# Kernel optimization log

Measured on AMD Instinct MI355X. Metric: run time of the kernel, lower is better.

The kernel has to match this reference:

```python
import jax, jax.numpy as jnp
import numpy as np

B, S, MSL, MQL = 512, 20, 32, 16
E, H, HQ = 32, 32, 32
V, A = 10000, 1000
D = H + S  # per-object feature dim (hidden + one-hot tag) = 52
G = 256


def _lstm_last_h(x, Wih, Whh, bih, bhh):
    # x: [N, T, E]; torch LSTM gate order i,f,g,o; returns final hidden [N, H]
    n, t, _ = x.shape
    h_dim = Whh.shape[1]
    xp = jnp.einsum('nte,ge->ntg', x, Wih) + bih + bhh  # precompute input projection

    def step(carry, xt):
        h, c = carry
        gates = xt + h @ Whh.T
        i, f, g, o = jnp.split(gates, 4, axis=-1)
        c = jax.nn.sigmoid(f) * c + jax.nn.sigmoid(i) * jnp.tanh(g)
        h = jax.nn.sigmoid(o) * jnp.tanh(c)
        return (h, c), None

    init = (jnp.zeros((n, h_dim), x.dtype), jnp.zeros((n, h_dim), x.dtype))
    (h, _), _ = jax.lax.scan(step, init, xp.transpose(1, 0, 2))
    return h


def setup_inputs() -> dict:
    key = jax.random.key(0)
    ks = jax.random.split(key, 24)
    nrm = lambda k, shp, std=0.1: (jax.random.normal(k, shp) * std).astype(jnp.float32)
    inp = {
        'story': jax.random.randint(ks[0], (B, S, MSL), 0, V),
        'question': jax.random.randint(ks[1], (B, MQL), 0, V),
        'emb': nrm(ks[2], (V, E)),
        's_Wih': nrm(ks[3], (4 * H, E)),
        's_Whh': nrm(ks[4], (4 * H, H)),
        's_bih': jnp.zeros((4 * H,), jnp.float32),
        's_bhh': jnp.zeros((4 * H,), jnp.float32),
        'q_Wih': nrm(ks[5], (4 * HQ, E)),
        'q_Whh': nrm(ks[6], (4 * HQ, HQ)),
        'q_bih': jnp.zeros((4 * HQ,), jnp.float32),
        'q_bhh': jnp.zeros((4 * HQ,), jnp.float32),
        'g1_w': nrm(ks[7], (G, 2 * D + HQ)), 'g1_b': jnp.zeros((G,), jnp.float32),
        'g2_w': nrm(ks[8], (G, G)), 'g2_b': jnp.zeros((G,), jnp.float32),
        'g3_w': nrm(ks[9], (G, G)), 'g3_b': jnp.zeros((G,), jnp.float32),
        'g4_w': nrm(ks[10], (G, G)), 'g4_b': jnp.zeros((G,), jnp.float32),
        'f1_w': nrm(ks[11], (G, G)), 'f1_b': jnp.zeros((G,), jnp.float32),
        'f2_w': nrm(ks[12], (512, G)), 'f2_b': jnp.zeros((512,), jnp.float32),
        'f3_w': nrm(ks[13], (A, 512)), 'f3_b': jnp.zeros((A,), jnp.float32),
    }
    return inp


def reference(story, question, emb, s_Wih, s_Whh, s_bih, s_bhh,
              q_Wih, q_Whh, q_bih, q_bhh,
              g1_w, g1_b, g2_w, g2_b, g3_w, g3_b, g4_w, g4_b,
              f1_w, f1_b, f2_w, f2_b, f3_w, f3_b):
    bsz = story.shape[0]
    # story encoding: LSTM over each sentence, take final hidden state
    s_emb = emb[story].reshape(bsz * S, MSL, E)
    s_state = _lstm_last_h(s_emb, s_Wih, s_Whh, s_bih, s_bhh).reshape(bsz, S, H)
    # append one-hot position tags -> story objects [B, S, H+S]
    tags = jnp.broadcast_to(jnp.eye(S, dtype=s_state.dtype), (bsz, S, S))
    obj = jnp.concatenate([s_state, tags], axis=2)
    # question encoding
    q_state = _lstm_last_h(emb[question], q_Wih, q_Whh, q_bih, q_bhh)  # [B, HQ]
    # g_theta over all S*S pairs: g1(cat(o_i, o_j, q)) split into three projections
    Wa, Wb, Wq = g1_w[:, :D], g1_w[:, D:2 * D], g1_w[:, 2 * D:]
    pi = jnp.einsum('bsd,gd->bsg', obj, Wa)   # object-as-first projection
    pj = jnp.einsum('bsd,gd->bsg', obj, Wb)   # object-as-second projection
    pq = q_state @ Wq.T                        # [B, G]
    x = jax.nn.relu(pi[:, :, None, :] + pj[:, None, :, :] + pq[:, None, None, :] + g1_b)  # [B,S,S,G]
    x = jax.nn.relu(jnp.einsum('bijg,hg->bijh', x, g2_w) + g2_b)
    x = jax.nn.relu(jnp.einsum('bijg,hg->bijh', x, g3_w) + g3_b)
    x = jax.nn.relu(jnp.einsum('bijg,hg->bijh', x, g4_w) + g4_b)
    sum_g = x.sum(axis=(1, 2))  # [B, G]
    out = jax.nn.relu(sum_g @ f1_w.T + f1_b)
    out = jax.nn.relu(out @ f2_w.T + f2_b)
    return out @ f3_w.T + f3_b
```

## Files before the change

### kernel.cpp

```cpp
#include <hip/hip_runtime.h>

typedef unsigned short u16;
typedef unsigned int   u32;
typedef __attribute__((ext_vector_type(8))) short short8;
typedef __attribute__((ext_vector_type(4))) float f32x4;

#define OFF_XPS   0
#define OFF_XPQ   1280000
#define OFF_QST   2560000
#define OFF_PI    2576384
#define OFF_PJ    5197824
#define OFF_QA    7819264
#define OFF_TGA   7950336
#define OFF_TGB   7955456
#define OFF_WB    7960576
#define OFF_STB   8058880
#define OFF_WAB   8222720
#define OFF_WBB   8226816
#define OFF_WHHS  8230912
#define OFF_WHHQ  8232960
#define OFF_WF1   8235008
#define OFF_WF2   8267776
#define OFF_WF3   8333312
#define OFF_SGP   0
#define OFF_ACT1  720896
#define OFF_ACT2  786432

__device__ __forceinline__ u16 f2bf(float f){
  union { float f; u32 u; } v; v.f = f;
  u32 u = v.u;
  u32 r = u + 0x7fffu + ((u >> 16) & 1u);
  return (u16)(r >> 16);
}
__device__ __forceinline__ u32 pack2(float a, float b){
  u32 r;
  asm("v_cvt_pk_bf16_f32 %0, %1, %2" : "=v"(r) : "v"(a), "v"(b));
  return r;
}
__device__ __forceinline__ float sigm(float x){
  return __builtin_amdgcn_rcpf(1.f + __expf(-x));
}

#define LBAR() do {                                        \
    asm volatile("s_waitcnt lgkmcnt(0)" ::: "memory");     \
    __builtin_amdgcn_s_barrier();                          \
    __builtin_amdgcn_sched_barrier(0);                     \
  } while (0)

__global__ __launch_bounds__(256) void prep_kernel(
    const float* __restrict__ emb,
    const float* __restrict__ swih, const float* __restrict__ sbih, const float* __restrict__ sbhh,
    const float* __restrict__ qwih, const float* __restrict__ qbih, const float* __restrict__ qbhh,
    const float* __restrict__ g2w, const float* __restrict__ g3w, const float* __restrict__ g4w,
    const float* __restrict__ g1w,
    const float* __restrict__ swhh, const float* __restrict__ qwhh,
    const float* __restrict__ f1w, const float* __restrict__ f2w, const float* __restrict__ f3w,
    float* __restrict__ xps, float* __restrict__ xpq,
    u16* __restrict__ wb, u16* __restrict__ wab, u16* __restrict__ wbb,
    float* __restrict__ tga, float* __restrict__ tgb,
    u16* __restrict__ whhbs, u16* __restrict__ whhbq,
    u16* __restrict__ wf1, u16* __restrict__ wf2, u16* __restrict__ wf3)
{
  __shared__ float wl[2048];
  __shared__ float bl[64];
  const int tid = threadIdx.x;
  if (blockIdx.y == 2){
    const int B = 196608;
    const int C = B + 16384;
    const int D = C + 10240;
    const int E = D + 8192;
    const int F = E + 65536;
    const int G = F + 131072;
    const int H = G + 524288;
    for (int idx = blockIdx.x*256 + tid; idx < H; idx += 160*256){
      if (idx < B){
        const int k = idx;
        const float* src = (k < 65536) ? g2w : ((k < 131072) ? g3w : g4w);
        wb[k] = f2bf(src[k & 65535]);
      } else if (idx < C){
        const int k = idx - B;
        if (k < 8192) wab[k] = f2bf(g1w[(k>>5)*136 + (k&31)]);
        else { const int k2 = k - 8192; wbb[k2] = f2bf(g1w[(k2>>5)*136 + 52 + (k2&31)]); }
      } else if (idx < D){
        const int k = idx - C;
        if (k < 5120){ const int s = k >> 8, g = k & 255; tga[k] = g1w[g*136 + 32 + s]; }
        else { const int k2 = k - 5120; const int s = k2 >> 8, g = k2 & 255; tgb[k2] = g1w[g*136 + 84 + s]; }
      } else if (idx < E){
        const int k = idx - D;
        if (k < 4096) whhbs[k] = f2bf(swhh[k]);
        else whhbq[k-4096] = f2bf(qwhh[k-4096]);
      } else if (idx < F){
        const int k = idx - E;
        wf1[k] = f2bf(f1w[k]);
      } else if (idx < G){
        const int k = idx - F;
        wf2[k] = f2bf(f2w[k]);
      } else {
        const int k = idx - G;
        const int o = k >> 9, kk = k & 511;
        wf3[k] = (o < 1000) ? f2bf(f3w[o*512 + kk]) : (u16)0;
      }
    }
    return;
  }
  if (blockIdx.x >= 80) return;
  const bool isq = blockIdx.y;
  const float* wih = isq ? qwih : swih;
  const float* bih = isq ? qbih : sbih;
  const float* bhh = isq ? qbhh : sbhh;
  float* xp = isq ? xpq : xps;
  const int gh = (blockIdx.x & 1) * 64;
  #pragma unroll
  for (int k=0;k<8;k++) wl[k*256+tid] = wih[gh*32 + k*256 + tid];
  if (tid < 64) bl[tid] = bih[gh+tid] + bhh[gh+tid];
  __syncthreads();
  const int v = (blockIdx.x >> 1)*256 + tid;
  if (v >= 10000) return;
  float4 e[8];
  #pragma unroll
  for (int q=0;q<8;q++) e[q] = *(const float4*)(emb + v*32 + q*4);
  for (int g2=0; g2<64; ++g2){
    const int g = gh + g2;
    float acc = bl[g2];
    #pragma unroll
    for (int q=0;q<8;q++){
      float4 w4 = *(const float4*)(&wl[g2*32 + q*4]);
      acc = fmaf(e[q].x, w4.x, acc); acc = fmaf(e[q].y, w4.y, acc);
      acc = fmaf(e[q].z, w4.z, acc); acc = fmaf(e[q].w, w4.w, acc);
    }
    xp[v*128 + (g&15)*8 + (g>>4)] = acc;
  }
}

template<int LEN>
__device__ __forceinline__ void lstm_mfma_run(
    const int* __restrict__ toks, int s0,
    const float* __restrict__ xpr, const u16* __restrict__ whhb,
    u16* __restrict__ hl, int lane, float* h0r, float* h1r)
{
  const int l15 = lane & 15, l4 = lane >> 4;
  short8 wf[8];
  #pragma unroll
  for (int f=0; f<8; f++)
    wf[f] = *(const short8*)(whhb + (f*16+l15)*32 + l4*8);
  short8 ha = (short8){0,0,0,0,0,0,0,0};
  float c0[4] = {0,0,0,0}, c1[4] = {0,0,0,0};
  int tk[4];
  #pragma unroll
  for (int r=0;r<4;r++) tk[r] = toks[(s0 + l4*4 + r)*LEN];
  float4 xa[4], xb[4];
  #pragma unroll
  for (int r=0;r<4;r++){
    xa[r] = *(const float4*)(xpr + tk[r]*128 + l15*8);
    xb[r] = *(const float4*)(xpr + tk[r]*128 + l15*8 + 4);
  }
  #pragma unroll
  for (int t=0; t<LEN; ++t){
    int tkn[4];
    if (t+1 < LEN){
      #pragma unroll
      for (int r=0;r<4;r++) tkn[r] = toks[(s0 + l4*4 + r)*LEN + t + 1];
    }
    const f32x4 z = (f32x4){0.f,0.f,0.f,0.f};
    f32x4 acc[8];
    #pragma unroll
    for (int f=0; f<8; f++)
      acc[f] = __builtin_amdgcn_mfma_f32_16x16x32_bf16(ha, wf[f], z, 0, 0, 0);
    float4 na[4], nb[4];
    if (t+1 < LEN){
      #pragma unroll
      for (int r=0;r<4;r++){
        na[r] = *(const float4*)(xpr + tkn[r]*128 + l15*8);
        nb[r] = *(const float4*)(xpr + tkn[r]*128 + l15*8 + 4);
      }
    }
    #pragma unroll
    for (int r=0;r<4;r++){
      float i0 = sigm(acc[0][r] + xa[r].x);
      float f0 = sigm(acc[2][r] + xa[r].z);
      float g0 = 2.f*sigm(2.f*(acc[4][r] + xb[r].x)) - 1.f;
      float o0 = sigm(acc[6][r] + xb[r].z);
      c0[r] = fmaf(f0, c0[r], i0*g0);
      h0r[r] = o0 * (2.f*sigm(2.f*c0[r]) - 1.f);
      float i1 = sigm(acc[1][r] + xa[r].y);
      float f1v = sigm(acc[3][r] + xa[r].w);
      float g1v = 2.f*sigm(2.f*(acc[5][r] + xb[r].y)) - 1.f;
      float o1 = sigm(acc[7][r] + xb[r].w);
      c1[r] = fmaf(f1v, c1[r], i1*g1v);
      h1r[r] = o1 * (2.f*sigm(2.f*c1[r]) - 1.f);
    }
    if (t+1 < LEN){
      #pragma unroll
      for (int r=0;r<4;r++){
        hl[(l4*4+r)*32 + l15]      = f2bf(h0r[r]);
        hl[(l4*4+r)*32 + 16 + l15] = f2bf(h1r[r]);
      }
      __syncthreads();
      ha = *(const short8*)(hl + l15*32 + l4*8);
      #pragma unroll
      for (int r=0;r<4;r++){ xa[r] = na[r]; xb[r] = nb[r]; }
    }
  }
}

__global__ __launch_bounds__(64) void lstm_kernel(
    const int* __restrict__ story, const int* __restrict__ question,
    const float* __restrict__ xprs, const float* __restrict__ xprq,
    const u16* __restrict__ whhbs, const u16* __restrict__ whhbq,
    u16* __restrict__ stb, float* __restrict__ qst)
{
  __shared__ u16 hl[512];
  const int lane = threadIdx.x;
  const int w = blockIdx.x;
  const int l15 = lane & 15, l4 = lane >> 4;
  float h0r[4], h1r[4];
  if (w >= 640){
    const int s0 = (w - 640)*16;
    lstm_mfma_run<16>(question, s0, xprq, whhbq, hl, lane, h0r, h1r);
    #pragma unroll
    for (int r=0;r<4;r++){
      qst[(s0 + l4*4 + r)*32 + l15]      = h0r[r];
      qst[(s0 + l4*4 + r)*32 + 16 + l15] = h1r[r];
    }
  } else {
    const int s0 = w*16;
    lstm_mfma_run<32>(story, s0, xprs, whhbs, hl, lane, h0r, h1r);
    #pragma unroll
    for (int r=0;r<4;r++){
      stb[(s0 + l4*4 + r)*32 + l15]      = f2bf(h0r[r]);
      stb[(s0 + l4*4 + r)*32 + 16 + l15] = f2bf(h1r[r]);
    }
  }
}

__global__ __launch_bounds__(256) void pipj_kernel(
    const u16* __restrict__ stb, const u16* __restrict__ wab, const u16* __restrict__ wbb,
    const float* __restrict__ tga, const float* __restrict__ tgb,
    const float* __restrict__ qst, const float* __restrict__ g1w, const float* __restrict__ g1b,
    float* __restrict__ pi, float* __restrict__ pj, float* __restrict__ qa)
{
  const int tid = threadIdx.x;
  if (blockIdx.y == 2){
    for (int idx = blockIdx.x*256 + tid; idx < 131072; idx += 160*256){
      const int b = idx >> 8, g = idx & 255;
      const float* qs = qst + b*32;
      const float* wr = g1w + g*136 + 104;
      float acc = g1b[g];
      #pragma unroll
      for (int q=0;q<8;q++){
        float4 s4 = *(const float4*)(qs + q*4);
        float4 w4 = *(const float4*)(wr + q*4);
        acc = fmaf(s4.x, w4.x, acc); acc = fmaf(s4.y, w4.y, acc);
        acc = fmaf(s4.z, w4.z, acc); acc = fmaf(s4.w, w4.w, acc);
      }
      qa[idx] = acc;
    }
    return;
  }
  const int lane = tid & 63;
  const int wv = tid >> 6;
  const int l15 = lane & 15;
  const int l4r = lane >> 4;
  const int bs0 = blockIdx.x * 64;
  const bool isj = blockIdx.y;
  const u16* wB = isj ? wbb : wab;
  const float* tg = isj ? tgb : tga;
  float* out = isj ? pj : pi;

  short8 af[4], bf[4];
  #pragma unroll
  for (int mf=0; mf<4; mf++)
    af[mf] = *(const short8*)(stb + (bs0 + mf*16 + l15)*32 + l4r*8);
  #pragma unroll
  for (int nf=0; nf<4; nf++)
    bf[nf] = *(const short8*)(wB + (wv*64 + nf*16 + l15)*32 + l4r*8);

  #pragma unroll
  for (int mf=0; mf<4; mf++){
    #pragma unroll
    for (int nf=0; nf<4; nf++){
      f32x4 acc = (f32x4){0.f,0.f,0.f,0.f};
      acc = __builtin_amdgcn_mfma_f32_16x16x32_bf16(af[mf], bf[nf], acc, 0, 0, 0);
      const int g = wv*64 + nf*16 + l15;
      #pragma unroll
      for (int r=0; r<4; r++){
        const int bs = bs0 + mf*16 + l4r*4 + r;
        const int s = bs % 20;
        out[bs*256 + g] = acc[r] + tg[s*256 + g];
      }
    }
  }
}

#define LDX 264
__global__ __launch_bounds__(512) void relnet_kernel(
    const float* __restrict__ pi, const float* __restrict__ pj, const float* __restrict__ qa,
    const u16* __restrict__ w2, const u16* __restrict__ w3, const u16* __restrict__ w4,
    const float* __restrict__ b2, const float* __restrict__ b3, const float* __restrict__ b4,
    float* __restrict__ sgp)
{
  __shared__ u16 Xs[80*LDX + 6656];
  const int tid = threadIdx.x;
  const int lane = tid & 63;
  const int wv  = tid >> 6;
  const int b   = blockIdx.x;
  const int t   = blockIdx.y;
  const int l15 = lane & 15;
  const int l4  = lane >> 4;

  const float* pib = pi + b*(20*256);
  const float* pjb = pj + b*(20*256);
  const float* qab = qa + b*256;

  const int ar0 = (wv*32 + l15)*256 + l4*8;
  const int ar1 = (wv*32 + 16 + l15)*256 + l4*8;

  #pragma unroll
  for (int it = 0; it < 5; ++it){
    int u  = it*512 + tid;
    int m  = u >> 5;
    int gq = (u & 31) << 3;
    int R  = t*80 + m;
    int i  = R / 20;
    int j  = R - i*20;
    const float4* pr = (const float4*)(pib + i*256 + gq);
    const float4* qr = (const float4*)(pjb + j*256 + gq);
    const float4* ar = (const float4*)(qab + gq);
    uint4 pk;
    {
      float4 a = pr[0], c4 = qr[0], d4 = ar[0];
      pk.x = pack2(fmaxf(a.x+c4.x+d4.x,0.f), fmaxf(a.y+c4.y+d4.y,0.f));
      pk.y = pack2(fmaxf(a.z+c4.z+d4.z,0.f), fmaxf(a.w+c4.w+d4.w,0.f));
    }
    {
      float4 a = pr[1], c4 = qr[1], d4 = ar[1];
      pk.z = pack2(fmaxf(a.x+c4.x+d4.x,0.f), fmaxf(a.y+c4.y+d4.y,0.f));
      pk.w = pack2(fmaxf(a.z+c4.z+d4.z,0.f), fmaxf(a.w+c4.w+d4.w,0.f));
    }
    *(uint4*)(&Xs[m*LDX + gq]) = pk;
  }

  short8 pf0 = *(const short8*)(w2 + ar0);
  short8 pf1 = *(const short8*)(w2 + ar1);

  LBAR();

  #pragma unroll
  for (int lay = 0; lay < 2; ++lay){
    const u16*   W    = lay ? w3 : w2;
    const u16*   Wn   = lay ? w4 : w3;
    const float* bias = lay ? b3 : b2;
    f32x4 acc[2][5];
    #pragma unroll
    for (int hf=0; hf<2; hf++)
      #pragma unroll
      for (int mf=0; mf<5; mf++)
        acc[hf][mf] = (f32x4){0.f,0.f,0.f,0.f};

    short8 xc[5];
    #pragma unroll
    for (int mf=0; mf<5; mf++)
      xc[mf] = *(const short8*)(&Xs[(mf*16 + l15)*LDX + l4*8]);

    #pragma unroll
    for (int kk = 0; kk < 8; ++kk){
      short8 a0 = pf0, a1 = pf1;
      const u16* src = (kk < 7) ? W : Wn;
      const int  kn  = (kk < 7) ? (kk+1)*32 : 0;
      pf0 = *(const short8*)(src + ar0 + kn);
      pf1 = *(const short8*)(src + ar1 + kn);
      short8 xn[5];
      if (kk < 7){
        #pragma unroll
        for (int mf=0; mf<5; mf++)
          xn[mf] = *(const short8*)(&Xs[(mf*16 + l15)*LDX + (kk+1)*32 + l4*8]);
      }
      __builtin_amdgcn_s_setprio(1);
      #pragma unroll
      for (int mf=0; mf<5; mf++){
        acc[0][mf] = __builtin_amdgcn_mfma_f32_16x16x32_bf16(a0, xc[mf], acc[0][mf], 0, 0, 0);
        acc[1][mf] = __builtin_amdgcn_mfma_f32_16x16x32_bf16(a1, xc[mf], acc[1][mf], 0, 0, 0);
      }
      __builtin_amdgcn_s_setprio(0);
      if (kk < 7){
        #pragma unroll
        for (int mf=0; mf<5; mf++) xc[mf] = xn[mf];
      }
    }

    LBAR();
    #pragma unroll
    for (int hf=0; hf<2; hf++){
      int h0 = wv*32 + hf*16 + l4*4;
      float4 bi = *(const float4*)(bias + h0);
      #pragma unroll
      for (int mf=0; mf<5; mf++){
        int m = mf*16 + l15;
        uint2 pk;
        pk.x = pack2(fmaxf(acc[hf][mf][0]+bi.x,0.f), fmaxf(acc[hf][mf][1]+bi.y,0.f));
        pk.y = pack2(fmaxf(acc[hf][mf][2]+bi.z,0.f), fmaxf(acc[hf][mf][3]+bi.w,0.f));
        *(uint2*)(&Xs[m*LDX + h0]) = pk;
      }
    }
    LBAR();
  }

  {
    f32x4 acc[2][5];
    #pragma unroll
    for (int hf=0; hf<2; hf++)
      #pragma unroll
      for (int mf=0; mf<5; mf++)
        acc[hf][mf] = (f32x4){0.f,0.f,0.f,0.f};

    short8 xc[5];
    #pragma unroll
    for (int mf=0; mf<5; mf++)
      xc[mf] = *(const short8*)(&Xs[(mf*16 + l15)*LDX + l4*8]);

    #pragma unroll
    for (int kk = 0; kk < 8; ++kk){
      short8 a0 = pf0, a1 = pf1;
      if (kk < 7){
        pf0 = *(const short8*)(w4 + ar0 + (kk+1)*32);
        pf1 = *(const short8*)(w4 + ar1 + (kk+1)*32);
      }
      short8 xn[5];
      if (kk < 7){
        #pragma unroll
        for (int mf=0; mf<5; mf++)
          xn[mf] = *(const short8*)(&Xs[(mf*16 + l15)*LDX + (kk+1)*32 + l4*8]);
      }
      __builtin_amdgcn_s_setprio(1);
      #pragma unroll
      for (int mf=0; mf<5; mf++){
        acc[0][mf] = __builtin_amdgcn_mfma_f32_16x16x32_bf16(a0, xc[mf], acc[0][mf], 0, 0, 0);
        acc[1][mf] = __builtin_amdgcn_mfma_f32_16x16x32_bf16(a1, xc[mf], acc[1][mf], 0, 0, 0);
      }
      __builtin_amdgcn_s_setprio(0);
      if (kk < 7){
        #pragma unroll
        for (int mf=0; mf<5; mf++) xc[mf] = xn[mf];
      }
    }

    #pragma unroll
    for (int hf=0; hf<2; hf++){
      int h0 = wv*32 + hf*16 + l4*4;
      float4 bi = *(const float4*)(b4 + h0);
      float s0 = 0.f, s1 = 0.f, s2 = 0.f, s3 = 0.f;
      #pragma unroll
      for (int mf=0; mf<5; mf++){
        s0 += fmaxf(acc[hf][mf][0]+bi.x,0.f);
        s1 += fmaxf(acc[hf][mf][1]+bi.y,0.f);
        s2 += fmaxf(acc[hf][mf][2]+bi.z,0.f);
        s3 += fmaxf(acc[hf][mf][3]+bi.w,0.f);
      }
      float sv[4] = {s0, s1, s2, s3};
      #pragma unroll
      for (int r=0; r<4; r++){
        float v = sv[r];
        v += __shfl_xor(v, 1);
        v += __shfl_xor(v, 2);
        v += __shfl_xor(v, 4);
        v += __shfl_xor(v, 8);
        if (l15 == 0){
          int h = h0 + r;
          sgp[t*131072 + b*256 + h] = v;
        }
      }
    }
  }
}

__global__ __launch_bounds__(256) void fcm1_kernel(
    const float* __restrict__ sgp, const u16* __restrict__ w,
    const float* __restrict__ bias, u16* __restrict__ outp)
{
  const int tid = threadIdx.x, lane = tid & 63, wv = tid >> 6;
  const int l15 = lane & 15, l4 = lane >> 4;
  const int b0 = blockIdx.x*16;
  const int of0 = blockIdx.y*4 + wv;
  f32x4 acc = (f32x4){0.f,0.f,0.f,0.f};
  #pragma unroll
  for (int kk=0; kk<8; ++kk){
    const float* base = sgp + (b0+l15)*256 + kk*32 + l4*8;
    float4 s0 = {0.f,0.f,0.f,0.f}, s1 = {0.f,0.f,0.f,0.f};
    #pragma unroll
    for (int t=0;t<5;t++){
      float4 a = *(const float4*)(base + t*131072);
      float4 c = *(const float4*)(base + t*131072 + 4);
      s0.x += a.x; s0.y += a.y; s0.z += a.z; s0.w += a.w;
      s1.x += c.x; s1.y += c.y; s1.z += c.z; s1.w += c.w;
    }
    union { short8 s; u32 u[4]; } xf;
    xf.u[0] = pack2(s0.x, s0.y); xf.u[1] = pack2(s0.z, s0.w);
    xf.u[2] = pack2(s1.x, s1.y); xf.u[3] = pack2(s1.z, s1.w);
    short8 af = *(const short8*)(w + (of0*16 + l15)*256 + kk*32 + l4*8);
    acc = __builtin_amdgcn_mfma_f32_16x16x32_bf16(af, xf.s, acc, 0, 0, 0);
  }
  const int b = b0 + l15;
  const int o0 = of0*16 + l4*4;
  float v0 = fmaxf(acc[0] + bias[o0+0], 0.f);
  float v1 = fmaxf(acc[1] + bias[o0+1], 0.f);
  float v2 = fmaxf(acc[2] + bias[o0+2], 0.f);
  float v3 = fmaxf(acc[3] + bias[o0+3], 0.f);
  uint2 pk;
  pk.x = pack2(v0, v1);
  pk.y = pack2(v2, v3);
  *(uint2*)(outp + (size_t)b*256 + o0) = pk;
}

template<int HF, int KK, int OPAD, int OREAL, int MODE>
__global__ __launch_bounds__(256) void fcm_kernel(
    const u16* __restrict__ in, const u16* __restrict__ w,
    const float* __restrict__ bias, void* __restrict__ outp)
{
  const int K = KK*32;
  const int tid = threadIdx.x, lane = tid & 63, wv = tid >> 6;
  const int l15 = lane & 15, l4 = lane >> 4;
  const int b0 = blockIdx.x*16;
  const int of0 = (blockIdx.y*4 + wv)*HF;
  f32x4 acc[HF];
  #pragma unroll
  for (int hf=0; hf<HF; hf++) acc[hf] = (f32x4){0.f,0.f,0.f,0.f};
  #pragma unroll 4
  for (int kk=0; kk<KK; ++kk){
    short8 xf = *(const short8*)(in + (b0+l15)*K + kk*32 + l4*8);
    #pragma unroll
    for (int hf=0; hf<HF; hf++){
      short8 af = *(const short8*)(w + ((of0+hf)*16 + l15)*K + kk*32 + l4*8);
      acc[hf] = __builtin_amdgcn_mfma_f32_16x16x32_bf16(af, xf, acc[hf], 0, 0, 0);
    }
  }
  const int b = b0 + l15;
  #pragma unroll
  for (int hf=0; hf<HF; hf++){
    const int o0 = (of0+hf)*16 + l4*4;
    float v[4];
    #pragma unroll
    for (int r=0;r<4;r++){
      float bv = (o0+r < OREAL) ? bias[o0+r] : 0.f;
      v[r] = acc[hf][r] + bv;
    }
    if (MODE == 0){
      uint2 pk;
      pk.x = pack2(fmaxf(v[0],0.f), fmaxf(v[1],0.f));
      pk.y = pack2(fmaxf(v[2],0.f), fmaxf(v[3],0.f));
      *(uint2*)((u16*)outp + (size_t)b*OPAD + o0) = pk;
    } else {
      float* of = (float*)outp;
      #pragma unroll
      for (int r=0;r<4;r++)
        if (o0+r < OREAL) of[(size_t)b*OREAL + o0 + r] = v[r];
    }
  }
}

extern "C" void kernel_launch(void* const* d_in, const int* in_sizes, int n_in,
                              void* d_out, int out_size, void* d_ws, size_t ws_size,
                              hipStream_t stream)
{
  const int*   story    = (const int*)d_in[0];
  const int*   question = (const int*)d_in[1];
  const float* emb   = (const float*)d_in[2];
  const float* s_wih = (const float*)d_in[3];
  const float* s_whh = (const float*)d_in[4];
  const float* s_bih = (const float*)d_in[5];
  const float* s_bhh = (const float*)d_in[6];
  const float* q_wih = (const float*)d_in[7];
  const float* q_whh = (const float*)d_in[8];
  const float* q_bih = (const float*)d_in[9];
  const float* q_bhh = (const float*)d_in[10];
  const float* g1w = (const float*)d_in[11];
  const float* g1b = (const float*)d_in[12];
  const float* g2w = (const float*)d_in[13];
  const float* g2b = (const float*)d_in[14];
  const float* g3w = (const float*)d_in[15];
  const float* g3b = (const float*)d_in[16];
  const float* g4w = (const float*)d_in[17];
  const float* g4b = (const float*)d_in[18];
  const float* f1w = (const float*)d_in[19];
  const float* f1b = (const float*)d_in[20];
  const float* f2w = (const float*)d_in[21];
  const float* f2b = (const float*)d_in[22];
  const float* f3w = (const float*)d_in[23];
  const float* f3b = (const float*)d_in[24];

  float* ws  = (float*)d_ws;
  float* xps = ws + OFF_XPS;
  float* xpq = ws + OFF_XPQ;
  float* qst = ws + OFF_QST;
  float* pi  = ws + OFF_PI;
  float* pj  = ws + OFF_PJ;
  float* qa  = ws + OFF_QA;
  float* tga = ws + OFF_TGA;
  float* tgb = ws + OFF_TGB;
  float* sgp = ws + OFF_SGP;
  u16*   wb    = (u16*)(ws + OFF_WB);
  u16*   w2b   = wb;
  u16*   w3b   = wb + 65536;
  u16*   w4b   = wb + 131072;
  u16*   stb   = (u16*)(ws + OFF_STB);
  u16*   wab   = (u16*)(ws + OFF_WAB);
  u16*   wbb   = (u16*)(ws + OFF_WBB);
  u16*   whhbs = (u16*)(ws + OFF_WHHS);
  u16*   whhbq = (u16*)(ws + OFF_WHHQ);
  u16*   wf1   = (u16*)(ws + OFF_WF1);
  u16*   wf2   = (u16*)(ws + OFF_WF2);
  u16*   wf3   = (u16*)(ws + OFF_WF3);
  u16*   act1  = (u16*)(ws + OFF_ACT1);
  u16*   act2  = (u16*)(ws + OFF_ACT2);

  prep_kernel<<<dim3(160,3), dim3(256), 0, stream>>>(
      emb, s_wih, s_bih, s_bhh, q_wih, q_bih, q_bhh,
      g2w, g3w, g4w, g1w, s_whh, q_whh, f1w, f2w, f3w,
      xps, xpq, wb, wab, wbb, tga, tgb, whhbs, whhbq, wf1, wf2, wf3);
  lstm_kernel<<<dim3(672), dim3(64), 0, stream>>>(
      story, question, xps, xpq, whhbs, whhbq, stb, qst);
  pipj_kernel<<<dim3(160,3), dim3(256), 0, stream>>>(
      stb, wab, wbb, tga, tgb, qst, g1w, g1b, pi, pj, qa);
  relnet_kernel<<<dim3(512,5), dim3(512), 0, stream>>>(
      pi, pj, qa, w2b, w3b, w4b, g2b, g3b, g4b, sgp);
  fcm1_kernel<<<dim3(32,4), dim3(256), 0, stream>>>(sgp, wf1, f1b, act1);
  fcm_kernel<2,8,512,512,0><<<dim3(32,4), dim3(256), 0, stream>>>(act1, wf2, f2b, act2);
  fcm_kernel<2,16,1024,1000,1><<<dim3(32,8), dim3(256), 0, stream>>>(act2, wf3, f3b, (float*)d_out);
}
```

Before: 231.6 us.

## Process two batch items per relnet block to reuse weight fragments

Each relnet block now handles two batch elements, with two shared-memory activation tiles and two accumulator sets, so every weight fragment loaded from global memory feeds twice as many MFMAs. The grid is halved to match. The old cross-layer weight prefetch and s_setprio hints are dropped, so weight loads are now issued inside each k-step. The extra accumulators raise register pressure and may lower occupancy, and halving the block count leaves fewer blocks for latency hiding.

Measured after the change: 202.7 us. -12.5%, faster.

```diff
diff --git a/kernel.cpp b/kernel.cpp
--- a/kernel.cpp
+++ b/kernel.cpp
@@ -299,92 +299,83 @@
     const float* __restrict__ b2, const float* __restrict__ b3, const float* __restrict__ b4,
     float* __restrict__ sgp)
 {
-  __shared__ u16 Xs[80*LDX + 6656];
+  __shared__ u16 Xs[2][80*LDX];
   const int tid = threadIdx.x;
   const int lane = tid & 63;
   const int wv  = tid >> 6;
-  const int b   = blockIdx.x;
+  const int bA  = blockIdx.x*2;
   const int t   = blockIdx.y;
   const int l15 = lane & 15;
   const int l4  = lane >> 4;
 
-  const float* pib = pi + b*(20*256);
-  const float* pjb = pj + b*(20*256);
-  const float* qab = qa + b*256;
-
   const int ar0 = (wv*32 + l15)*256 + l4*8;
   const int ar1 = (wv*32 + 16 + l15)*256 + l4*8;
 
   #pragma unroll
-  for (int it = 0; it < 5; ++it){
-    int u  = it*512 + tid;
-    int m  = u >> 5;
-    int gq = (u & 31) << 3;
-    int R  = t*80 + m;
-    int i  = R / 20;
-    int j  = R - i*20;
-    const float4* pr = (const float4*)(pib + i*256 + gq);
-    const float4* qr = (const float4*)(pjb + j*256 + gq);
-    const float4* ar = (const float4*)(qab + gq);
-    uint4 pk;
-    {
-      float4 a = pr[0], c4 = qr[0], d4 = ar[0];
-      pk.x = pack2(fmaxf(a.x+c4.x+d4.x,0.f), fmaxf(a.y+c4.y+d4.y,0.f));
-      pk.y = pack2(fmaxf(a.z+c4.z+d4.z,0.f), fmaxf(a.w+c4.w+d4.w,0.f));
-    }
-    {
-      float4 a = pr[1], c4 = qr[1], d4 = ar[1];
-      pk.z = pack2(fmaxf(a.x+c4.x+d4.x,0.f), fmaxf(a.y+c4.y+d4.y,0.f));
-      pk.w = pack2(fmaxf(a.z+c4.z+d4.z,0.f), fmaxf(a.w+c4.w+d4.w,0.f));
-    }
-    *(uint4*)(&Xs[m*LDX + gq]) = pk;
-  }
-
-  short8 pf0 = *(const short8*)(w2 + ar0);
-  short8 pf1 = *(const short8*)(w2 + ar1);
-
+  for (int s = 0; s < 2; ++s){
+    const float* pib = pi + (bA+s)*(20*256);
+    const float* pjb = pj + (bA+s)*(20*256);
+    const float* qab = qa + (bA+s)*256;
+    #pragma unroll
+    for (int it = 0; it < 5; ++it){
+      int u  = it*512 + tid;
+      int m  = u >> 5;
+      int gq = (u & 31) << 3;
+      int R  = t*80 + m;
+      int i  = R / 20;
+      int j  = R - i*20;
+      const float4* pr = (const float4*)(pib + i*256 + gq);
+      const float4* qr = (const float4*)(pjb + j*256 + gq);
+      const float4* ar = (const float4*)(qab + gq);
+      uint4 pk;
+      {
+        float4 a = pr[0], c4 = qr[0], d4 = ar[0];
+        pk.x = pack2(fmaxf(a.x+c4.x+d4.x,0.f), fmaxf(a.y+c4.y+d4.y,0.f));
+        pk.y = pack2(fmaxf(a.z+c4.z+d4.z,0.f), fmaxf(a.w+c4.w+d4.w,0.f));
+      }
+      {
+        float4 a = pr[1], c4 = qr[1], d4 = ar[1];
+        pk.z = pack2(fmaxf(a.x+c4.x+d4.x,0.f), fmaxf(a.y+c4.y+d4.y,0.f));
+        pk.w = pack2(fmaxf(a.z+c4.z+d4.z,0.f), fmaxf(a.w+c4.w+d4.w,0.f));
+      }
+      *(uint4*)(&Xs[s][m*LDX + gq]) = pk;
+    }
+  }
   LBAR();
 
   #pragma unroll
   for (int lay = 0; lay < 2; ++lay){
     const u16*   W    = lay ? w3 : w2;
-    const u16*   Wn   = lay ? w4 : w3;
     const float* bias = lay ? b3 : b2;
-    f32x4 acc[2][5];
+    f32x4 aA[2][5], aB[2][5];
     #pragma unroll
     for (int hf=0; hf<2; hf++)
       #pragma unroll
+      for (int mf=0; mf<5; mf++){
+        aA[hf][mf] = (f32x4){0.f,0.f,0.f,0.f};
+        aB[hf][mf] = (f32x4){0.f,0.f,0.f,0.f};
+      }
+
+    #pragma unroll
+    for (int kk = 0; kk < 8; ++kk){
+      short8 w0 = *(const short8*)(W + ar0 + kk*32);
+      short8 w1 = *(const short8*)(W + ar1 + kk*32);
+      short8 xA[5], xB[5];
+      #pragma unroll
       for (int mf=0; mf<5; mf++)
-        acc[hf][mf] = (f32x4){0.f,0.f,0.f,0.f};
-
-    short8 xc[5];
-    #pragma unroll
-    for (int mf=0; mf<5; mf++)
-      xc[mf] = *(const short8*)(&Xs[(mf*16 + l15)*LDX + l4*8]);
-
-    #pragma unroll
-    for (int kk = 0; kk < 8; ++kk){
-      short8 a0 = pf0, a1 = pf1;
-      const u16* src = (kk < 7) ? W : Wn;
-      const int  kn  = (kk < 7) ? (kk+1)*32 : 0;
-      pf0 = *(const short8*)(src + ar0 + kn);
-      pf1 = *(const short8*)(src + ar1 + kn);
-      short8 xn[5];
-      if (kk < 7){
-        #pragma unroll
-        for (int mf=0; mf<5; mf++)
-          xn[mf] = *(const short8*)(&Xs[(mf*16 + l15)*LDX + (kk+1)*32 + l4*8]);
-      }
-      __builtin_amdgcn_s_setprio(1);
-      #pragma unroll
-      for (int mf=0; mf<5; mf++){
-        acc[0][mf] = __builtin_amdgcn_mfma_f32_16x16x32_bf16(a0, xc[mf], acc[0][mf], 0, 0, 0);
-        acc[1][mf] = __builtin_amdgcn_mfma_f32_16x16x32_bf16(a1, xc[mf], acc[1][mf], 0, 0, 0);
-      }
-      __builtin_amdgcn_s_setprio(0);
-      if (kk < 7){
-        #pragma unroll
-        for (int mf=0; mf<5; mf++) xc[mf] = xn[mf];
+        xA[mf] = *(const short8*)(&Xs[0][(mf*16 + l15)*LDX + kk*32 + l4*8]);
+      #pragma unroll
+      for (int mf=0; mf<5; mf++)
+        xB[mf] = *(const short8*)(&Xs[1][(mf*16 + l15)*LDX + kk*32 + l4*8]);
+      #pragma unroll
+      for (int mf=0; mf<5; mf++){
+        aA[0][mf] = __builtin_amdgcn_mfma_f32_16x16x32_bf16(w0, xA[mf], aA[0][mf], 0, 0, 0);
+        aA[1][mf] = __builtin_amdgcn_mfma_f32_16x16x32_bf16(w1, xA[mf], aA[1][mf], 0, 0, 0);
+      }
+      #pragma unroll
+      for (int mf=0; mf<5; mf++){
+        aB[0][mf] = __builtin_amdgcn_mfma_f32_16x16x32_bf16(w0, xB[mf], aB[0][mf], 0, 0, 0);
+        aB[1][mf] = __builtin_amdgcn_mfma_f32_16x16x32_bf16(w1, xB[mf], aB[1][mf], 0, 0, 0);
       }
     }
 
@@ -396,51 +387,48 @@
       #pragma unroll
       for (int mf=0; mf<5; mf++){
         int m = mf*16 + l15;
-        uint2 pk;
-        pk.x = pack2(fmaxf(acc[hf][mf][0]+bi.x,0.f), fmaxf(acc[hf][mf][1]+bi.y,0.f));
-        pk.y = pack2(fmaxf(acc[hf][mf][2]+bi.z,0.f), fmaxf(acc[hf][mf][3]+bi.w,0.f));
-        *(uint2*)(&Xs[m*LDX + h0]) = pk;
+        uint2 pkA, pkB;
+        pkA.x = pack2(fmaxf(aA[hf][mf][0]+bi.x,0.f), fmaxf(aA[hf][mf][1]+bi.y,0.f));
+        pkA.y = pack2(fmaxf(aA[hf][mf][2]+bi.z,0.f), fmaxf(aA[hf][mf][3]+bi.w,0.f));
+        *(uint2*)(&Xs[0][m*LDX + h0]) = pkA;
+        pkB.x = pack2(fmaxf(aB[hf][mf][0]+bi.x,0.f), fmaxf(aB[hf][mf][1]+bi.y,0.f));
+        pkB.y = pack2(fmaxf(aB[hf][mf][2]+bi.z,0.f), fmaxf(aB[hf][mf][3]+bi.w,0.f));
+        *(uint2*)(&Xs[1][m*LDX + h0]) = pkB;
       }
     }
     LBAR();
   }
 
   {
-    f32x4 acc[2][5];
+    f32x4 aA[2][5], aB[2][5];
     #pragma unroll
     for (int hf=0; hf<2; hf++)
       #pragma unroll
+      for (int mf=0; mf<5; mf++){
+        aA[hf][mf] = (f32x4){0.f,0.f,0.f,0.f};
+        aB[hf][mf] = (f32x4){0.f,0.f,0.f,0.f};
+      }
+
+    #pragma unroll
+    for (int kk = 0; kk < 8; ++kk){
+      short8 w0 = *(const short8*)(w4 + ar0 + kk*32);
+      short8 w1 = *(const short8*)(w4 + ar1 + kk*32);
+      short8 xA[5], xB[5];
+      #pragma unroll
       for (int mf=0; mf<5; mf++)
-        acc[hf][mf] = (f32x4){0.f,0.f,0.f,0.f};
-
-    short8 xc[5];
-    #pragma unroll
-    for (int mf=0; mf<5; mf++)
-      xc[mf] = *(const short8*)(&Xs[(mf*16 + l15)*LDX + l4*8]);
-
-    #pragma unroll
-    for (int kk = 0; kk < 8; ++kk){
-      short8 a0 = pf0, a1 = pf1;
-      if (kk < 7){
-        pf0 = *(const short8*)(w4 + ar0 + (kk+1)*32);
-        pf1 = *(const short8*)(w4 + ar1 + (kk+1)*32);
-      }
-      short8 xn[5];
-      if (kk < 7){
-        #pragma unroll
-        for (int mf=0; mf<5; mf++)
-          xn[mf] = *(const short8*)(&Xs[(mf*16 + l15)*LDX + (kk+1)*32 + l4*8]);
-      }
-      __builtin_amdgcn_s_setprio(1);
-      #pragma unroll
-      for (int mf=0; mf<5; mf++){
-        acc[0][mf] = __builtin_amdgcn_mfma_f32_16x16x32_bf16(a0, xc[mf], acc[0][mf], 0, 0, 0);
-        acc[1][mf] = __builtin_amdgcn_mfma_f32_16x16x32_bf16(a1, xc[mf], acc[1][mf], 0, 0, 0);
-      }
-      __builtin_amdgcn_s_setprio(0);
-      if (kk < 7){
-        #pragma unroll
-        for (int mf=0; mf<5; mf++) xc[mf] = xn[mf];
+        xA[mf] = *(const short8*)(&Xs[0][(mf*16 + l15)*LDX + kk*32 + l4*8]);
+      #pragma unroll
+      for (int mf=0; mf<5; mf++)
+        xB[mf] = *(const short8*)(&Xs[1][(mf*16 + l15)*LDX + kk*32 + l4*8]);
+      #pragma unroll
+      for (int mf=0; mf<5; mf++){
+        aA[0][mf] = __builtin_amdgcn_mfma_f32_16x16x32_bf16(w0, xA[mf], aA[0][mf], 0, 0, 0);
+        aA[1][mf] = __builtin_amdgcn_mfma_f32_16x16x32_bf16(w1, xA[mf], aA[1][mf], 0, 0, 0);
+      }
+      #pragma unroll
+      for (int mf=0; mf<5; mf++){
+        aB[0][mf] = __builtin_amdgcn_mfma_f32_16x16x32_bf16(w0, xB[mf], aB[0][mf], 0, 0, 0);
+        aB[1][mf] = __builtin_amdgcn_mfma_f32_16x16x32_bf16(w1, xB[mf], aB[1][mf], 0, 0, 0);
       }
     }
 
@@ -448,25 +436,35 @@
     for (int hf=0; hf<2; hf++){
       int h0 = wv*32 + hf*16 + l4*4;
       float4 bi = *(const float4*)(b4 + h0);
-      float s0 = 0.f, s1 = 0.f, s2 = 0.f, s3 = 0.f;
-      #pragma unroll
-      for (int mf=0; mf<5; mf++){
-        s0 += fmaxf(acc[hf][mf][0]+bi.x,0.f);
-        s1 += fmaxf(acc[hf][mf][1]+bi.y,0.f);
-        s2 += fmaxf(acc[hf][mf][2]+bi.z,0.f);
-        s3 += fmaxf(acc[hf][mf][3]+bi.w,0.f);
-      }
-      float sv[4] = {s0, s1, s2, s3};
+      float sA[4] = {0.f,0.f,0.f,0.f};
+      float sB[4] = {0.f,0.f,0.f,0.f};
+      #pragma unroll
+      for (int mf=0; mf<5; mf++){
+        sA[0] += fmaxf(aA[hf][mf][0]+bi.x,0.f);
+        sA[1] += fmaxf(aA[hf][mf][1]+bi.y,0.f);
+        sA[2] += fmaxf(aA[hf][mf][2]+bi.z,0.f);
+        sA[3] += fmaxf(aA[hf][mf][3]+bi.w,0.f);
+        sB[0] += fmaxf(aB[hf][mf][0]+bi.x,0.f);
+        sB[1] += fmaxf(aB[hf][mf][1]+bi.y,0.f);
+        sB[2] += fmaxf(aB[hf][mf][2]+bi.z,0.f);
+        sB[3] += fmaxf(aB[hf][mf][3]+bi.w,0.f);
+      }
       #pragma unroll
       for (int r=0; r<4; r++){
-        float v = sv[r];
-        v += __shfl_xor(v, 1);
-        v += __shfl_xor(v, 2);
-        v += __shfl_xor(v, 4);
-        v += __shfl_xor(v, 8);
+        float vA = sA[r];
+        vA += __shfl_xor(vA, 1);
+        vA += __shfl_xor(vA, 2);
+        vA += __shfl_xor(vA, 4);
+        vA += __shfl_xor(vA, 8);
+        float vB = sB[r];
+        vB += __shfl_xor(vB, 1);
+        vB += __shfl_xor(vB, 2);
+        vB += __shfl_xor(vB, 4);
+        vB += __shfl_xor(vB, 8);
         if (l15 == 0){
           int h = h0 + r;
-          sgp[t*131072 + b*256 + h] = v;
+          sgp[t*131072 + bA*256 + h]       = vA;
+          sgp[t*131072 + (bA+1)*256 + h]   = vB;
         }
       }
     }
@@ -620,7 +618,7 @@
       story, question, xps, xpq, whhbs, whhbq, stb, qst);
   pipj_kernel<<<dim3(160,3), dim3(256), 0, stream>>>(
       stb, wab, wbb, tga, tgb, qst, g1w, g1b, pi, pj, qa);
-  relnet_kernel<<<dim3(512,5), dim3(512), 0, stream>>>(
+  relnet_kernel<<<dim3(256,5), dim3(512), 0, stream>>>(
       pi, pj, qa, w2b, w3b, w4b, g2b, g3b, g4b, sgp);
   fcm1_kernel<<<dim3(32,4), dim3(256), 0, stream>>>(sgp, wf1, f1b, act1);
   fcm_kernel<2,8,512,512,0><<<dim3(32,4), dim3(256), 0, stream>>>(act1, wf2, f2b, act2);
```

## Process all pair tiles per batch in one block to reuse weight fragments

Applied to the files above, without the earlier changes.

The relation-network kernel now launches one block per batch element instead of five. Each block handles the 400 pairs in two passes of three and two 80-row tiles. Each weight fragment loaded from global memory is reused across several tiles, cutting redundant weight traffic. The cost is fewer blocks (512 versus 2560), more LDS per block (three tiles), more accumulator registers (up to 120 f32x4 per thread), and loss of the software prefetch and setprio scheduling, so occupancy and latency hiding may drop.

Result: faster. 205.8 us (-11.2%).

```diff
diff --git a/kernel.cpp b/kernel.cpp
--- a/kernel.cpp
+++ b/kernel.cpp
@@ -293,184 +293,181 @@
 }
 
 #define LDX 264
+#define TSZ (80*LDX)
+
+template<int NT>
+__device__ __forceinline__ void relnet_pass(
+    int b, int t0, u16* __restrict__ Xs,
+    const float* __restrict__ pi, const float* __restrict__ pj, const float* __restrict__ qa,
+    const u16* __restrict__ w2, const u16* __restrict__ w3, const u16* __restrict__ w4,
+    const float* __restrict__ b2, const float* __restrict__ b3, const float* __restrict__ b4,
+    float* __restrict__ sgp,
+    int tid, int wv, int l15, int l4, int ar0, int ar1)
+{
+  const float* pib = pi + b*(20*256);
+  const float* pjb = pj + b*(20*256);
+  const float* qab = qa + b*256;
+
+  #pragma unroll
+  for (int s = 0; s < NT; ++s){
+    const int tt = t0 + s;
+    #pragma unroll
+    for (int it = 0; it < 5; ++it){
+      int ux = it*512 + tid;
+      int m  = ux >> 5;
+      int gq = (ux & 31) << 3;
+      int R  = tt*80 + m;
+      int i  = R / 20;
+      int j  = R - i*20;
+      const float4* pr = (const float4*)(pib + i*256 + gq);
+      const float4* qr = (const float4*)(pjb + j*256 + gq);
+      const float4* ar = (const float4*)(qab + gq);
+      uint4 pk;
+      {
+        float4 a = pr[0], c4 = qr[0], d4 = ar[0];
+        pk.x = pack2(fmaxf(a.x+c4.x+d4.x,0.f), fmaxf(a.y+c4.y+d4.y,0.f));
+        pk.y = pack2(fmaxf(a.z+c4.z+d4.z,0.f), fmaxf(a.w+c4.w+d4.w,0.f));
+      }
+      {
+        float4 a = pr[1], c4 = qr[1], d4 = ar[1];
+        pk.z = pack2(fmaxf(a.x+c4.x+d4.x,0.f), fmaxf(a.y+c4.y+d4.y,0.f));
+        pk.w = pack2(fmaxf(a.z+c4.z+d4.z,0.f), fmaxf(a.w+c4.w+d4.w,0.f));
+      }
+      *(uint4*)(&Xs[s*TSZ + m*LDX + gq]) = pk;
+    }
+  }
+  LBAR();
+
+  #pragma unroll
+  for (int lay = 0; lay < 2; ++lay){
+    const u16*   W    = lay ? w3 : w2;
+    const float* bias = lay ? b3 : b2;
+    f32x4 acc[NT][2][5];
+    #pragma unroll
+    for (int s=0; s<NT; s++)
+      #pragma unroll
+      for (int hf=0; hf<2; hf++)
+        #pragma unroll
+        for (int mf=0; mf<5; mf++)
+          acc[s][hf][mf] = (f32x4){0.f,0.f,0.f,0.f};
+
+    #pragma unroll
+    for (int kk = 0; kk < 8; ++kk){
+      short8 w0 = *(const short8*)(W + ar0 + kk*32);
+      short8 w1 = *(const short8*)(W + ar1 + kk*32);
+      #pragma unroll
+      for (int s=0; s<NT; s++){
+        short8 xf[5];
+        #pragma unroll
+        for (int mf=0; mf<5; mf++)
+          xf[mf] = *(const short8*)(&Xs[s*TSZ + (mf*16 + l15)*LDX + kk*32 + l4*8]);
+        #pragma unroll
+        for (int mf=0; mf<5; mf++){
+          acc[s][0][mf] = __builtin_amdgcn_mfma_f32_16x16x32_bf16(w0, xf[mf], acc[s][0][mf], 0, 0, 0);
+          acc[s][1][mf] = __builtin_amdgcn_mfma_f32_16x16x32_bf16(w1, xf[mf], acc[s][1][mf], 0, 0, 0);
+        }
+      }
+    }
+
+    LBAR();
+    #pragma unroll
+    for (int hf=0; hf<2; hf++){
+      int h0 = wv*32 + hf*16 + l4*4;
+      float4 bi = *(const float4*)(bias + h0);
+      #pragma unroll
+      for (int mf=0; mf<5; mf++){
+        int m = mf*16 + l15;
+        #pragma unroll
+        for (int s=0; s<NT; s++){
+          uint2 pk;
+          pk.x = pack2(fmaxf(acc[s][hf][mf][0]+bi.x,0.f), fmaxf(acc[s][hf][mf][1]+bi.y,0.f));
+          pk.y = pack2(fmaxf(acc[s][hf][mf][2]+bi.z,0.f), fmaxf(acc[s][hf][mf][3]+bi.w,0.f));
+          *(uint2*)(&Xs[s*TSZ + m*LDX + h0]) = pk;
+        }
+      }
+    }
+    LBAR();
+  }
+
+  {
+    f32x4 acc[NT][2][5];
+    #pragma unroll
+    for (int s=0; s<NT; s++)
+      #pragma unroll
+      for (int hf=0; hf<2; hf++)
+        #pragma unroll
+        for (int mf=0; mf<5; mf++)
+          acc[s][hf][mf] = (f32x4){0.f,0.f,0.f,0.f};
+
+    #pragma unroll
+    for (int kk = 0; kk < 8; ++kk){
+      short8 w0 = *(const short8*)(w4 + ar0 + kk*32);
+      short8 w1 = *(const short8*)(w4 + ar1 + kk*32);
+      #pragma unroll
+      for (int s=0; s<NT; s++){
+        short8 xf[5];
+        #pragma unroll
+        for (int mf=0; mf<5; mf++)
+          xf[mf] = *(const short8*)(&Xs[s*TSZ + (mf*16 + l15)*LDX + kk*32 + l4*8]);
+        #pragma unroll
+        for (int mf=0; mf<5; mf++){
+          acc[s][0][mf] = __builtin_amdgcn_mfma_f32_16x16x32_bf16(w0, xf[mf], acc[s][0][mf], 0, 0, 0);
+          acc[s][1][mf] = __builtin_amdgcn_mfma_f32_16x16x32_bf16(w1, xf[mf], acc[s][1][mf], 0, 0, 0);
+        }
+      }
+    }
+
+    #pragma unroll
+    for (int hf=0; hf<2; hf++){
+      int h0 = wv*32 + hf*16 + l4*4;
+      float4 bi = *(const float4*)(b4 + h0);
+      #pragma unroll
+      for (int s=0; s<NT; s++){
+        float s0 = 0.f, s1 = 0.f, s2 = 0.f, s3 = 0.f;
+        #pragma unroll
+        for (int mf=0; mf<5; mf++){
+          s0 += fmaxf(acc[s][hf][mf][0]+bi.x,0.f);
+          s1 += fmaxf(acc[s][hf][mf][1]+bi.y,0.f);
+          s2 += fmaxf(acc[s][hf][mf][2]+bi.z,0.f);
+          s3 += fmaxf(acc[s][hf][mf][3]+bi.w,0.f);
+        }
+        float sv[4] = {s0, s1, s2, s3};
+        #pragma unroll
+        for (int r=0; r<4; r++){
+          float v = sv[r];
+          v += __shfl_xor(v, 1); v += __shfl_xor(v, 2);
+          v += __shfl_xor(v, 4); v += __shfl_xor(v, 8);
+          if (l15 == 0){
+            int h = h0 + r;
+            sgp[(t0+s)*131072 + b*256 + h] = v;
+          }
+        }
+      }
+    }
+  }
+}
+
 __global__ __launch_bounds__(512) void relnet_kernel(
     const float* __restrict__ pi, const float* __restrict__ pj, const float* __restrict__ qa,
     const u16* __restrict__ w2, const u16* __restrict__ w3, const u16* __restrict__ w4,
     const float* __restrict__ b2, const float* __restrict__ b3, const float* __restrict__ b4,
     float* __restrict__ sgp)
 {
-  __shared__ u16 Xs[80*LDX + 6656];
+  __shared__ u16 Xs[3*TSZ];
   const int tid = threadIdx.x;
   const int lane = tid & 63;
   const int wv  = tid >> 6;
-  const int b   = blockIdx.x;
-  const int t   = blockIdx.y;
   const int l15 = lane & 15;
   const int l4  = lane >> 4;
-
-  const float* pib = pi + b*(20*256);
-  const float* pjb = pj + b*(20*256);
-  const float* qab = qa + b*256;
-
+  const int b   = blockIdx.x;
   const int ar0 = (wv*32 + l15)*256 + l4*8;
   const int ar1 = (wv*32 + 16 + l15)*256 + l4*8;
 
-  #pragma unroll
-  for (int it = 0; it < 5; ++it){
-    int u  = it*512 + tid;
-    int m  = u >> 5;
-    int gq = (u & 31) << 3;
-    int R  = t*80 + m;
-    int i  = R / 20;
-    int j  = R - i*20;
-    const float4* pr = (const float4*)(pib + i*256 + gq);
-    const float4* qr = (const float4*)(pjb + j*256 + gq);
-    const float4* ar = (const float4*)(qab + gq);
-    uint4 pk;
-    {
-      float4 a = pr[0], c4 = qr[0], d4 = ar[0];
-      pk.x = pack2(fmaxf(a.x+c4.x+d4.x,0.f), fmaxf(a.y+c4.y+d4.y,0.f));
-      pk.y = pack2(fmaxf(a.z+c4.z+d4.z,0.f), fmaxf(a.w+c4.w+d4.w,0.f));
-    }
-    {
-      float4 a = pr[1], c4 = qr[1], d4 = ar[1];
-      pk.z = pack2(fmaxf(a.x+c4.x+d4.x,0.f), fmaxf(a.y+c4.y+d4.y,0.f));
-      pk.w = pack2(fmaxf(a.z+c4.z+d4.z,0.f), fmaxf(a.w+c4.w+d4.w,0.f));
-    }
-    *(uint4*)(&Xs[m*LDX + gq]) = pk;
-  }
-
-  short8 pf0 = *(const short8*)(w2 + ar0);
-  short8 pf1 = *(const short8*)(w2 + ar1);
-
+  relnet_pass<3>(b, 0, Xs, pi, pj, qa, w2, w3, w4, b2, b3, b4, sgp,
+                 tid, wv, l15, l4, ar0, ar1);
   LBAR();
-
-  #pragma unroll
-  for (int lay = 0; lay < 2; ++lay){
-    const u16*   W    = lay ? w3 : w2;
-    const u16*   Wn   = lay ? w4 : w3;
-    const float* bias = lay ? b3 : b2;
-    f32x4 acc[2][5];
-    #pragma unroll
-    for (int hf=0; hf<2; hf++)
-      #pragma unroll
-      for (int mf=0; mf<5; mf++)
-        acc[hf][mf] = (f32x4){0.f,0.f,0.f,0.f};
-
-    short8 xc[5];
-    #pragma unroll
-    for (int mf=0; mf<5; mf++)
-      xc[mf] = *(const short8*)(&Xs[(mf*16 + l15)*LDX + l4*8]);
-
-    #pragma unroll
-    for (int kk = 0; kk < 8; ++kk){
-      short8 a0 = pf0, a1 = pf1;
-      const u16* src = (kk < 7) ? W : Wn;
-      const int  kn  = (kk < 7) ? (kk+1)*32 : 0;
-      pf0 = *(const short8*)(src + ar0 + kn);
-      pf1 = *(const short8*)(src + ar1 + kn);
-      short8 xn[5];
-      if (kk < 7){
-        #pragma unroll
-        for (int mf=0; mf<5; mf++)
-          xn[mf] = *(const short8*)(&Xs[(mf*16 + l15)*LDX + (kk+1)*32 + l4*8]);
-      }
-      __builtin_amdgcn_s_setprio(1);
-      #pragma unroll
-      for (int mf=0; mf<5; mf++){
-        acc[0][mf] = __builtin_amdgcn_mfma_f32_16x16x32_bf16(a0, xc[mf], acc[0][mf], 0, 0, 0);
-        acc[1][mf] = __builtin_amdgcn_mfma_f32_16x16x32_bf16(a1, xc[mf], acc[1][mf], 0, 0, 0);
-      }
-      __builtin_amdgcn_s_setprio(0);
-      if (kk < 7){
-        #pragma unroll
-        for (int mf=0; mf<5; mf++) xc[mf] = xn[mf];
-      }
-    }
-
-    LBAR();
-    #pragma unroll
-    for (int hf=0; hf<2; hf++){
-      int h0 = wv*32 + hf*16 + l4*4;
-      float4 bi = *(const float4*)(bias + h0);
-      #pragma unroll
-      for (int mf=0; mf<5; mf++){
-        int m = mf*16 + l15;
-        uint2 pk;
-        pk.x = pack2(fmaxf(acc[hf][mf][0]+bi.x,0.f), fmaxf(acc[hf][mf][1]+bi.y,0.f));
-        pk.y = pack2(fmaxf(acc[hf][mf][2]+bi.z,0.f), fmaxf(acc[hf][mf][3]+bi.w,0.f));
-        *(uint2*)(&Xs[m*LDX + h0]) = pk;
-      }
-    }
-    LBAR();
-  }
-
-  {
-    f32x4 acc[2][5];
-    #pragma unroll
-    for (int hf=0; hf<2; hf++)
-      #pragma unroll
-      for (int mf=0; mf<5; mf++)
-        acc[hf][mf] = (f32x4){0.f,0.f,0.f,0.f};
-
-    short8 xc[5];
-    #pragma unroll
-    for (int mf=0; mf<5; mf++)
-      xc[mf] = *(const short8*)(&Xs[(mf*16 + l15)*LDX + l4*8]);
-
-    #pragma unroll
-    for (int kk = 0; kk < 8; ++kk){
-      short8 a0 = pf0, a1 = pf1;
-      if (kk < 7){
-        pf0 = *(const short8*)(w4 + ar0 + (kk+1)*32);
-        pf1 = *(const short8*)(w4 + ar1 + (kk+1)*32);
-      }
-      short8 xn[5];
-      if (kk < 7){
-        #pragma unroll
-        for (int mf=0; mf<5; mf++)
-          xn[mf] = *(const short8*)(&Xs[(mf*16 + l15)*LDX + (kk+1)*32 + l4*8]);
-      }
-      __builtin_amdgcn_s_setprio(1);
-      #pragma unroll
-      for (int mf=0; mf<5; mf++){
-        acc[0][mf] = __builtin_amdgcn_mfma_f32_16x16x32_bf16(a0, xc[mf], acc[0][mf], 0, 0, 0);
-        acc[1][mf] = __builtin_amdgcn_mfma_f32_16x16x32_bf16(a1, xc[mf], acc[1][mf], 0, 0, 0);
-      }
-      __builtin_amdgcn_s_setprio(0);
-      if (kk < 7){
-        #pragma unroll
-        for (int mf=0; mf<5; mf++) xc[mf] = xn[mf];
-      }
-    }
-
-    #pragma unroll
-    for (int hf=0; hf<2; hf++){
-      int h0 = wv*32 + hf*16 + l4*4;
-      float4 bi = *(const float4*)(b4 + h0);
-      float s0 = 0.f, s1 = 0.f, s2 = 0.f, s3 = 0.f;
-      #pragma unroll
-      for (int mf=0; mf<5; mf++){
-        s0 += fmaxf(acc[hf][mf][0]+bi.x,0.f);
-        s1 += fmaxf(acc[hf][mf][1]+bi.y,0.f);
-        s2 += fmaxf(acc[hf][mf][2]+bi.z,0.f);
-        s3 += fmaxf(acc[hf][mf][3]+bi.w,0.f);
-      }
-      float sv[4] = {s0, s1, s2, s3};
-      #pragma unroll
-      for (int r=0; r<4; r++){
-        float v = sv[r];
-        v += __shfl_xor(v, 1);
-        v += __shfl_xor(v, 2);
-        v += __shfl_xor(v, 4);
-        v += __shfl_xor(v, 8);
-        if (l15 == 0){
-          int h = h0 + r;
-          sgp[t*131072 + b*256 + h] = v;
-        }
-      }
-    }
-  }
+  relnet_pass<2>(b, 3, Xs, pi, pj, qa, w2, w3, w4, b2, b3, b4, sgp,
+                 tid, wv, l15, l4, ar0, ar1);
 }
 
 __global__ __launch_bounds__(256) void fcm1_kernel(
@@ -620,7 +617,7 @@
       story, question, xps, xpq, whhbs, whhbq, stb, qst);
   pipj_kernel<<<dim3(160,3), dim3(256), 0, stream>>>(
       stb, wab, wbb, tga, tgb, qst, g1w, g1b, pi, pj, qa);
-  relnet_kernel<<<dim3(512,5), dim3(512), 0, stream>>>(
+  relnet_kernel<<<dim3(512), dim3(512), 0, stream>>>(
       pi, pj, qa, w2b, w3b, w4b, g2b, g3b, g4b, sgp);
   fcm1_kernel<<<dim3(32,4), dim3(256), 0, stream>>>(sgp, wf1, f1b, act1);
   fcm_kernel<2,8,512,512,0><<<dim3(32,4), dim3(256), 0, stream>>>(act1, wf2, f2b, act2);
```
